# Performance work log

Measured on AMD Instinct MI355X. Metric: run time of the kernel, lower is better.

## Reference

```python
import jax, jax.numpy as jnp
import numpy as np


def _dw_conv(x, w, ks):
    # x: [1, B*k, H, W], w: [B*k, 1, ks, ks], groups = B*k depthwise conv
    pad = (ks - 1) // 2
    return jax.lax.conv_general_dilated(
        x, w, window_strides=(1, 1), padding=[(pad, pad), (pad, pad)],
        feature_group_count=x.shape[1],
        dimension_numbers=('NCHW', 'OIHW', 'NCHW'))


def setup_inputs() -> dict:
    key = jax.random.key(0)
    ks = jax.random.split(key, 12)
    B, Cin, M, O, H, W = 8, 256, 256, 256, 128, 128
    k = 128  # static top-k channel count (eval-mode: ceil(M * clamp(mean(scores),0.25,1.0)) ~ M/2)
    inp = {
        'x': jax.random.normal(ks[0], (B, Cin, H, W), jnp.float32),
        'pw1_w': jax.random.normal(ks[1], (M, Cin), jnp.float32) * 0.02,
        'pw1_b': jnp.zeros((M,), jnp.float32),
        'fc1_w': jax.random.normal(ks[2], (2 * M, M), jnp.float32) * 0.02,
        'fc1_b': jnp.zeros((2 * M,), jnp.float32),
        'fc2_w': jax.random.normal(ks[3], (M, 2 * M), jnp.float32) * 0.02,
        'fc2_b': jnp.zeros((M,), jnp.float32),
        'off_w': jax.random.normal(ks[4], (6, M), jnp.float32) * 0.02,
        'off_b': jnp.zeros((6,), jnp.float32),
        'dw3': jax.random.normal(ks[5], (M, 1, 3, 3), jnp.float32) * 0.1,
        'dw5': jax.random.normal(ks[6], (M, 1, 5, 5), jnp.float32) * 0.1,
        'dw7': jax.random.normal(ks[7], (M, 1, 7, 7), jnp.float32) * 0.1,
        'pw_w': jax.random.normal(ks[8], (O, 3 * M), jnp.float32) * 0.02,
        'pw_b': jnp.zeros((O,), jnp.float32),
        'k': k,
    }
    return inp


def reference(x, pw1_w, pw1_b, fc1_w, fc1_b, fc2_w, fc2_b, off_w, off_b,
              dw3, dw5, dw7, pw_w, pw_b, k):
    B, _, H, W = x.shape
    residual = x  # identity shortcut (stride=1, in==out)
    # pointwise_1 (1x1 conv)
    h = jnp.einsum('bchw,oc->bohw', x, pw1_w) + pw1_b[None, :, None, None]
    # WidthPredictor (eval mode): scores from GAP of pre-ReLU features
    gap = h.mean(axis=(2, 3))                                   # [B, M]
    hid = jax.nn.relu(gap @ fc1_w.T + fc1_b)
    scores = jax.nn.sigmoid(hid @ fc2_w.T + fc2_b)              # [B, M]
    _, idx = jax.lax.top_k(scores, k)                           # [B, k]
    mask = jnp.zeros_like(scores).at[jnp.arange(B)[:, None], idx].set(1.0)
    h = jax.nn.relu(h)
    # offset generator: GAP -> 1x1 conv -> tanh
    gap2 = h.mean(axis=(2, 3))
    offsets = jnp.tanh(gap2 @ off_w.T + off_b).reshape(B, 3, 2)  # [B, branches, 2]
    # mask then take first k channels (as in original: (x*mask)[:, :k])
    sel = (h * mask[:, :, None, None])[:, :k]                    # [B, k, H, W]
    conv_in = sel.reshape(1, B * k, H, W)
    outs = []
    for i, (ksz, base) in enumerate([(3, dw3), (5, dw5), (7, dw7)]):
        scale = jax.nn.sigmoid(offsets[:, i, 0]).reshape(B, 1, 1, 1, 1)
        shift = jnp.tanh(offsets[:, i, 1]).reshape(B, 1, 1, 1, 1)
        w = base[:k][None] * (1.0 + scale) + shift               # [B, k, 1, ks, ks]
        y = _dw_conv(conv_in, w.reshape(B * k, 1, ksz, ksz), ksz)
        outs.append(y.reshape(B, k, H, W))
    fused = jnp.concatenate(outs, axis=1)                        # [B, 3k, H, W]
    sel_pw = pw_w[:, :3 * k]                                     # [O, 3k]
    out = jnp.einsum('bchw,oc->bohw', fused, sel_pw) + pw_b[None, :, None, None]
    return out + residual
```

## Files before the change

### kernel.cpp

```cpp
#include <hip/hip_runtime.h>
#include <math.h>

constexpr int B  = 8;
constexpr int C  = 256;
constexpr int M  = 256;
constexpr int O  = 256;
constexpr int H  = 128;
constexpr int W  = 128;
constexpr int HW = H * W;
constexpr int K  = 128;

using f16  = _Float16;
using f16x8 = __attribute__((ext_vector_type(8))) _Float16;
using f32x4 = __attribute__((ext_vector_type(4))) float;

constexpr size_t WS_MEANX = 0;
constexpr size_t WS_MASK  = 2048;
constexpr size_t WS_G2    = 4096;
constexpr size_t WS_OFF   = 6144;
constexpr size_t WS_WE3   = 6208;
constexpr size_t WS_WE5   = 15424;
constexpr size_t WS_WE7   = 41024;
constexpr size_t WS_WT1F  = 91200;
constexpr size_t WS_WT2F  = 123968;
constexpr size_t WS_SELH  = 173120;
constexpr size_t WS_YH    = 8561728;

__global__ __launch_bounds__(256) void kA(const float* __restrict__ x,
                                          float* __restrict__ ws) {
  float* meanx   = ws + WS_MEANX;
  float* gap2sum = ws + WS_G2;
  int plane = blockIdx.x;
  const float* p = x + (size_t)plane * HW;
  float s = 0.f;
  for (int i = threadIdx.x; i < HW / 4; i += 256) {
    float4 v = ((const float4*)p)[i];
    s += v.x + v.y + v.z + v.w;
  }
  __shared__ float red[256];
  red[threadIdx.x] = s;
  __syncthreads();
  for (int off = 128; off > 0; off >>= 1) {
    if (threadIdx.x < off) red[threadIdx.x] += red[threadIdx.x + off];
    __syncthreads();
  }
  if (threadIdx.x == 0) meanx[plane] = red[0] * (1.f / HW);
  if (blockIdx.x < 8) gap2sum[blockIdx.x * 256 + threadIdx.x] = 0.f;
}

__global__ __launch_bounds__(256) void kT(const float* __restrict__ pw1_w,
                                          const float* __restrict__ pw_w,
                                          float* __restrict__ ws) {
  f16* wt1f = (f16*)(ws + WS_WT1F);
  f16* wt2f = (f16*)(ws + WS_WT2F);
  int t = blockIdx.x * 256 + threadIdx.x;
  if (t < C * M) wt1f[t] = (f16)pw1_w[t];
  if (t < 384 * O) {
    int o = t / 384, cc = t % 384;
    wt2f[t] = (f16)pw_w[(size_t)o * 768 + cc];
  }
}

__global__ __launch_bounds__(256) void kB(const float* __restrict__ pw1_w,
                                          const float* __restrict__ pw1_b,
                                          const float* __restrict__ fc1_w,
                                          const float* __restrict__ fc1_b,
                                          const float* __restrict__ fc2_w,
                                          const float* __restrict__ fc2_b,
                                          float* __restrict__ ws) {
  int b = blockIdx.x;
  const float* meanx = ws + WS_MEANX + b * C;
  float* maskg = ws + WS_MASK;
  __shared__ float s_gap[M];
  __shared__ float s_hid[512];
  __shared__ float s_sc[M];
  int t = threadIdx.x;
  int lane = t & 63, wv = t >> 6;

  float4 mx = ((const float4*)meanx)[lane];
  for (int o0 = wv * 64; o0 < wv * 64 + 64; o0 += 4) {
    float s[4];
#pragma unroll
    for (int j = 0; j < 4; j++) {
      float4 w = ((const float4*)(pw1_w + (size_t)(o0 + j) * C))[lane];
      s[j] = mx.x * w.x + mx.y * w.y + mx.z * w.z + mx.w * w.w;
    }
#pragma unroll
    for (int off = 32; off > 0; off >>= 1)
#pragma unroll
      for (int j = 0; j < 4; j++) s[j] += __shfl_xor(s[j], off, 64);
    if (lane == 0) {
#pragma unroll
      for (int j = 0; j < 4; j++) s_gap[o0 + j] = s[j] + pw1_b[o0 + j];
    }
  }
  __syncthreads();

  float4 g4 = ((const float4*)s_gap)[lane];
  for (int j0 = wv * 128; j0 < wv * 128 + 128; j0 += 4) {
    float s[4];
#pragma unroll
    for (int j = 0; j < 4; j++) {
      float4 w = ((const float4*)(fc1_w + (size_t)(j0 + j) * M))[lane];
      s[j] = g4.x * w.x + g4.y * w.y + g4.z * w.z + g4.w * w.w;
    }
#pragma unroll
    for (int off = 32; off > 0; off >>= 1)
#pragma unroll
      for (int j = 0; j < 4; j++) s[j] += __shfl_xor(s[j], off, 64);
    if (lane == 0) {
#pragma unroll
      for (int j = 0; j < 4; j++) {
        float v = s[j] + fc1_b[j0 + j];
        s_hid[j0 + j] = v > 0.f ? v : 0.f;
      }
    }
  }
  __syncthreads();

  float4 h0 = ((const float4*)s_hid)[lane];
  float4 h1 = ((const float4*)s_hid)[lane + 64];
  for (int o0 = wv * 64; o0 < wv * 64 + 64; o0 += 4) {
    float s[4];
#pragma unroll
    for (int j = 0; j < 4; j++) {
      const float4* wr = (const float4*)(fc2_w + (size_t)(o0 + j) * 512);
      float4 w0 = wr[lane];
      float4 w1 = wr[lane + 64];
      s[j] = h0.x * w0.x + h0.y * w0.y + h0.z * w0.z + h0.w * w0.w +
             h1.x * w1.x + h1.y * w1.y + h1.z * w1.z + h1.w * w1.w;
    }
#pragma unroll
    for (int off = 32; off > 0; off >>= 1)
#pragma unroll
      for (int j = 0; j < 4; j++) s[j] += __shfl_xor(s[j], off, 64);
    if (lane == 0) {
#pragma unroll
      for (int j = 0; j < 4; j++) {
        float v = s[j] + fc2_b[o0 + j];
        s_sc[o0 + j] = 1.f / (1.f + expf(-v));
      }
    }
  }
  __syncthreads();

  {
    int j = t;
    float sj = s_sc[j];
    int cnt = 0;
    for (int m = 0; m < M; m++) {
      float sm = s_sc[m];
      cnt += (sm > sj) || (sm == sj && m < j);
    }
    maskg[b * M + j] = (cnt < K) ? 1.f : 0.f;
  }
}

__global__ __launch_bounds__(256) void kCm(const float* __restrict__ x,
                                           const float* __restrict__ pw1_b,
                                           float* __restrict__ ws) {
  const f16* wt1f = (const f16*)(ws + WS_WT1F);
  float* gap2sum  = ws + WS_G2;
  f16* selh       = (f16*)(ws + WS_SELH);
  int b  = blockIdx.z;
  int p0 = blockIdx.x * 64;
  __shared__ f16 Af[256 * 32];
  __shared__ f16 Bf[64 * 32];

  int t = threadIdx.x, l = t & 63, w = t >> 6;
  int q = l >> 4, n = l & 15;
  const float* xb = x + (size_t)b * C * HW;

  f32x4 acc[4][4];
#pragma unroll
  for (int i = 0; i < 4; i++)
#pragma unroll
    for (int j = 0; j < 4; j++)
#pragma unroll
      for (int r = 0; r < 4; r++) acc[i][j][r] = 0.f;

  for (int k0 = 0; k0 < C; k0 += 32) {
#pragma unroll
    for (int i = 0; i < 4; i++) {
      int ch = t + i * 256;
      int mt = ch >> 6, qq = (ch >> 4) & 3, m = ch & 15;
      f16x8 v = *(const f16x8*)&wt1f[(size_t)(mt * 16 + m) * C + k0 + qq * 8];
      ((f16x8*)Af)[ch] = v;
    }
    {
      int ch = t;
      int nt = ch >> 6, qq = (ch >> 4) & 3, nn = ch & 15;
      int p = p0 + nt * 16 + nn;
      f16x8 fr;
#pragma unroll
      for (int j = 0; j < 8; j++)
        fr[j] = (f16)xb[(size_t)(k0 + qq * 8 + j) * HW + p];
      ((f16x8*)Bf)[ch] = fr;
    }
    __syncthreads();
    f16x8 bfr[4], afr[4];
#pragma unroll
    for (int nt = 0; nt < 4; nt++) bfr[nt] = ((const f16x8*)Bf)[nt * 64 + l];
#pragma unroll
    for (int mt = 0; mt < 4; mt++) afr[mt] = ((const f16x8*)Af)[(w * 4 + mt) * 64 + l];
#pragma unroll
    for (int mt = 0; mt < 4; mt++)
#pragma unroll
      for (int nt = 0; nt < 4; nt++)
        acc[mt][nt] = __builtin_amdgcn_mfma_f32_16x16x32_f16(afr[mt], bfr[nt],
                                                             acc[mt][nt], 0, 0, 0);
    __syncthreads();
  }

#pragma unroll
  for (int mt = 0; mt < 4; mt++) {
    float rsum[4] = {0.f, 0.f, 0.f, 0.f};
    int obase = w * 64 + mt * 16 + q * 4;
    float bias[4];
#pragma unroll
    for (int r = 0; r < 4; r++) bias[r] = pw1_b[obase + r];
#pragma unroll
    for (int nt = 0; nt < 4; nt++) {
      int p = p0 + nt * 16 + n;
#pragma unroll
      for (int r = 0; r < 4; r++) {
        float h = acc[mt][nt][r] + bias[r];
        h = h > 0.f ? h : 0.f;
        rsum[r] += h;
        int o = obase + r;
        if (o < K) selh[((size_t)(b * K + o)) * HW + p] = (f16)h;
      }
    }
#pragma unroll
    for (int off = 1; off < 16; off <<= 1)
#pragma unroll
      for (int r = 0; r < 4; r++) rsum[r] += __shfl_xor(rsum[r], off, 64);
    if (n == 0) {
#pragma unroll
      for (int r = 0; r < 4; r++)
        atomicAdd(&gap2sum[b * M + obase + r], rsum[r]);
    }
  }
}

__global__ __launch_bounds__(256) void kD1(const float* __restrict__ off_w,
                                           const float* __restrict__ off_b,
                                           float* __restrict__ ws) {
  const float* gap2sum = ws + WS_G2;
  float* offv = ws + WS_OFF;
  __shared__ float s_off[48];
  int t = threadIdx.x;
  int lane = t & 63, wv = t >> 6;
  for (int id = wv; id < 48; id += 4) {
    int b = id / 6, j = id % 6;
    float4 g = ((const float4*)(gap2sum + b * M))[lane];
    float4 w = ((const float4*)(off_w + (size_t)j * M))[lane];
    float s = (g.x * w.x + g.y * w.y + g.z * w.z + g.w * w.w) * (1.f / HW);
#pragma unroll
    for (int off = 32; off > 0; off >>= 1) s += __shfl_xor(s, off, 64);
    if (lane == 0) s_off[id] = tanhf(s + off_b[j]);
  }
  __syncthreads();
  if (t < 24) {
    int b = t / 3, i = t % 3;
    offv[t]      = 1.f + 1.f / (1.f + expf(-s_off[b * 6 + 2 * i]));
    offv[24 + t] = tanhf(s_off[b * 6 + 2 * i + 1]);
  }
}

__global__ __launch_bounds__(256) void kD2(const float* __restrict__ dw3,
                                           const float* __restrict__ dw5,
                                           const float* __restrict__ dw7,
                                           float* __restrict__ ws) {
  const float* offv  = ws + WS_OFF;
  const float* maskg = ws + WS_MASK;
  float* wE3 = ws + WS_WE3;
  float* wE5 = ws + WS_WE5;
  float* wE7 = ws + WS_WE7;
  int tid = blockIdx.x * 256 + threadIdx.x;
  int stride = gridDim.x * 256;
  for (int i = tid; i < B * K * 9; i += stride) {
    int b = i / (K * 9), rem = i % (K * 9), c = rem / 9;
    wE3[i] = (dw3[rem] * offv[b * 3 + 0] + offv[24 + b * 3 + 0]) * maskg[b * M + c];
  }
  for (int i = tid; i < B * K * 25; i += stride) {
    int b = i / (K * 25), rem = i % (K * 25), c = rem / 25;
    wE5[i] = (dw5[rem] * offv[b * 3 + 1] + offv[24 + b * 3 + 1]) * maskg[b * M + c];
  }
  for (int i = tid; i < B * K * 49; i += stride) {
    int b = i / (K * 49), rem = i % (K * 49), c = rem / 49;
    wE7[i] = (dw7[rem] * offv[b * 3 + 2] + offv[24 + b * 3 + 2]) * maskg[b * M + c];
  }
}

__global__ __launch_bounds__(256) void kEm(const float* __restrict__ ws_ro,
                                           float* __restrict__ ws) {
  constexpr int SH = 38, SW = 134;
  __shared__ float sm[SH][SW];
  const f16* selh = (const f16*)(ws_ro + WS_SELH);
  f16* yh         = (f16*)(ws + WS_YH);
  int blk = blockIdx.x;
  int chunk = blk & 3;
  int plane = blk >> 2;
  int b = plane >> 7, c = plane & 127;
  int r0 = chunk * 32;
  const f16* in = selh + (size_t)plane * HW;
  for (int i = threadIdx.x; i < SH * SW; i += 256) {
    int rr = i / SW, cc = i % SW;
    int gy = r0 - 3 + rr, gx = cc - 3;
    float v = 0.f;
    if (gy >= 0 && gy < H && gx >= 0 && gx < W) v = (float)in[gy * W + gx];
    sm[rr][cc] = v;
  }
  __syncthreads();
  int col   = threadIdx.x & 127;
  int rhalf = threadIdx.x >> 7;

  const float* wE[3] = {ws_ro + WS_WE3 + (size_t)plane * 9,
                        ws_ro + WS_WE5 + (size_t)plane * 25,
                        ws_ro + WS_WE7 + (size_t)plane * 49};

#define CONV_BRANCH(KS, BR)                                                    \
  {                                                                            \
    constexpr int P = (KS - 1) / 2;                                            \
    float w[KS * KS];                                                          \
    _Pragma("unroll") for (int i = 0; i < KS * KS; i++) w[i] = wE[BR][i];      \
    float acc[16];                                                             \
    _Pragma("unroll") for (int r = 0; r < 16; r++) acc[r] = 0.f;               \
    _Pragma("unroll") for (int iy = 0; iy < 16 + 2 * P; iy++) {                \
      float v[KS];                                                             \
      _Pragma("unroll") for (int dx = 0; dx < KS; dx++)                        \
          v[dx] = sm[rhalf * 16 + iy + (3 - P)][col + (3 - P) + dx];           \
      _Pragma("unroll") for (int rr = 0; rr < 16; rr++) {                      \
        int dy = iy - rr;                                                      \
        if (dy >= 0 && dy < KS) {                                              \
          _Pragma("unroll") for (int dx = 0; dx < KS; dx++)                    \
              acc[rr] += v[dx] * w[dy * KS + dx];                              \
        }                                                                      \
      }                                                                        \
    }                                                                          \
    f16* outp = yh + ((size_t)(BR * B + b) * K + c) * HW;                      \
    _Pragma("unroll") for (int rr = 0; rr < 16; rr++)                          \
        outp[(size_t)(r0 + rhalf * 16 + rr) * W + col] = (f16)acc[rr];         \
  }

  CONV_BRANCH(3, 0)
  CONV_BRANCH(5, 1)
  CONV_BRANCH(7, 2)
#undef CONV_BRANCH
}

__global__ __launch_bounds__(256) void kFm(const float* __restrict__ x,
                                           const float* __restrict__ pw_b,
                                           const float* __restrict__ ws,
                                           float* __restrict__ out) {
  const f16* wt2f = (const f16*)(ws + WS_WT2F);
  const f16* yh   = (const f16*)(ws + WS_YH);
  int b  = blockIdx.z;
  int p0 = blockIdx.x * 64;
  __shared__ f16 Af[256 * 32];
  __shared__ f16 Bf[64 * 32];

  int t = threadIdx.x, l = t & 63, w = t >> 6;
  int q = l >> 4, n = l & 15;

  f32x4 acc[4][4];
#pragma unroll
  for (int i = 0; i < 4; i++)
#pragma unroll
    for (int j = 0; j < 4; j++)
#pragma unroll
      for (int r = 0; r < 4; r++) acc[i][j][r] = 0.f;

  for (int k0 = 0; k0 < 384; k0 += 32) {
    int br = k0 >> 7, kk = k0 & 127;
    const f16* ybr = yh + (size_t)(br * B + b) * K * HW;
#pragma unroll
    for (int i = 0; i < 4; i++) {
      int ch = t + i * 256;
      int mt = ch >> 6, qq = (ch >> 4) & 3, m = ch & 15;
      f16x8 v = *(const f16x8*)&wt2f[(size_t)(mt * 16 + m) * 384 + k0 + qq * 8];
      ((f16x8*)Af)[ch] = v;
    }
    {
      int ch = t;
      int nt = ch >> 6, qq = (ch >> 4) & 3, nn = ch & 15;
      int p = p0 + nt * 16 + nn;
      f16x8 fr;
#pragma unroll
      for (int j = 0; j < 8; j++)
        fr[j] = ybr[(size_t)(kk + qq * 8 + j) * HW + p];
      ((f16x8*)Bf)[ch] = fr;
    }
    __syncthreads();
    f16x8 bfr[4], afr[4];
#pragma unroll
    for (int nt = 0; nt < 4; nt++) bfr[nt] = ((const f16x8*)Bf)[nt * 64 + l];
#pragma unroll
    for (int mt = 0; mt < 4; mt++) afr[mt] = ((const f16x8*)Af)[(w * 4 + mt) * 64 + l];
#pragma unroll
    for (int mt = 0; mt < 4; mt++)
#pragma unroll
      for (int nt = 0; nt < 4; nt++)
        acc[mt][nt] = __builtin_amdgcn_mfma_f32_16x16x32_f16(afr[mt], bfr[nt],
                                                             acc[mt][nt], 0, 0, 0);
    __syncthreads();
  }

#pragma unroll
  for (int mt = 0; mt < 4; mt++) {
    int obase = w * 64 + mt * 16 + q * 4;
    float bias[4];
#pragma unroll
    for (int r = 0; r < 4; r++) bias[r] = pw_b[obase + r];
#pragma unroll
    for (int nt = 0; nt < 4; nt++) {
      int p = p0 + nt * 16 + n;
#pragma unroll
      for (int r = 0; r < 4; r++) {
        size_t idx = ((size_t)b * O + obase + r) * HW + p;
        out[idx] = acc[mt][nt][r] + bias[r] + x[idx];
      }
    }
  }
}

extern "C" void kernel_launch(void* const* d_in, const int* in_sizes, int n_in,
                              void* d_out, int out_size, void* d_ws, size_t ws_size,
                              hipStream_t stream) {
  const float* x     = (const float*)d_in[0];
  const float* pw1_w = (const float*)d_in[1];
  const float* pw1_b = (const float*)d_in[2];
  const float* fc1_w = (const float*)d_in[3];
  const float* fc1_b = (const float*)d_in[4];
  const float* fc2_w = (const float*)d_in[5];
  const float* fc2_b = (const float*)d_in[6];
  const float* off_w = (const float*)d_in[7];
  const float* off_b = (const float*)d_in[8];
  const float* dw3   = (const float*)d_in[9];
  const float* dw5   = (const float*)d_in[10];
  const float* dw7   = (const float*)d_in[11];
  const float* pw_w  = (const float*)d_in[12];
  const float* pw_b  = (const float*)d_in[13];
  float* out = (float*)d_out;
  float* ws  = (float*)d_ws;

  kA<<<B * C, 256, 0, stream>>>(x, ws);
  kT<<<384, 256, 0, stream>>>(pw1_w, pw_w, ws);
  kB<<<B, 256, 0, stream>>>(pw1_w, pw1_b, fc1_w, fc1_b, fc2_w, fc2_b, ws);
  kCm<<<dim3(HW / 64, 1, B), 256, 0, stream>>>(x, pw1_b, ws);
  kD1<<<1, 256, 0, stream>>>(off_w, off_b, ws);
  kD2<<<84, 256, 0, stream>>>(dw3, dw5, dw7, ws);
  kEm<<<B * K * 4, 256, 0, stream>>>(ws, ws);
  kFm<<<dim3(HW / 64, 1, B), 256, 0, stream>>>(x, pw_b, ws, out);
}
```

Baseline: 649.4 us.

## Vectorize and prefetch GEMM tile loads into registers with swizzled B layout

Both pointwise GEMM kernels (kCm and kFm) now load the B operand with row-contiguous vector loads instead of strided scalar loads that walk channels. Tiles are stored to LDS in an XOR-swizzled layout and transposed on the LDS read side. The next k-slice of A and B is prefetched into registers while the MFMAs for the current slice run, a software pipeline that overlaps global latency with compute. The cost is scalar LDS reads for the B fragments and more register pressure.

```diff
diff --git a/kernel.cpp b/kernel.cpp
--- a/kernel.cpp
+++ b/kernel.cpp
@@ -171,6 +171,18 @@
   int q = l >> 4, n = l & 15;
   const float* xb = x + (size_t)b * C * HW;
 
+  int crow = t >> 3;
+  int oct  = t & 7;
+  int qc_s = (crow >> 3) & 3;
+  int posB = crow * 64 + (((oct >> 1) ^ qc_s) << 4) + (oct & 1) * 8;
+
+  int aoff[4];
+#pragma unroll
+  for (int i = 0; i < 4; i++) {
+    int ch = t + i * 256;
+    aoff[i] = ((ch >> 6) * 16 + (ch & 15)) * C + ((ch >> 4) & 3) * 8;
+  }
+
   f32x4 acc[4][4];
 #pragma unroll
   for (int i = 0; i < 4; i++)
@@ -179,28 +191,41 @@
 #pragma unroll
       for (int r = 0; r < 4; r++) acc[i][j][r] = 0.f;
 
+  f16x8 rA[4];
+  float4 rB0, rB1;
+  auto loadA = [&](int k0) {
+#pragma unroll
+    for (int i = 0; i < 4; i++) rA[i] = *(const f16x8*)&wt1f[aoff[i] + k0];
+  };
+  auto loadB = [&](int k0) {
+    const float* bs = xb + (size_t)(k0 + crow) * HW + p0 + oct * 8;
+    rB0 = ((const float4*)bs)[0];
+    rB1 = ((const float4*)bs)[1];
+  };
+  loadA(0);
+  loadB(0);
+
   for (int k0 = 0; k0 < C; k0 += 32) {
-#pragma unroll
-    for (int i = 0; i < 4; i++) {
-      int ch = t + i * 256;
-      int mt = ch >> 6, qq = (ch >> 4) & 3, m = ch & 15;
-      f16x8 v = *(const f16x8*)&wt1f[(size_t)(mt * 16 + m) * C + k0 + qq * 8];
-      ((f16x8*)Af)[ch] = v;
-    }
+    __syncthreads();
+#pragma unroll
+    for (int i = 0; i < 4; i++) ((f16x8*)Af)[t + i * 256] = rA[i];
     {
-      int ch = t;
-      int nt = ch >> 6, qq = (ch >> 4) & 3, nn = ch & 15;
-      int p = p0 + nt * 16 + nn;
-      f16x8 fr;
-#pragma unroll
-      for (int j = 0; j < 8; j++)
-        fr[j] = (f16)xb[(size_t)(k0 + qq * 8 + j) * HW + p];
-      ((f16x8*)Bf)[ch] = fr;
-    }
+      f16x8 bv;
+      bv[0] = (f16)rB0.x; bv[1] = (f16)rB0.y; bv[2] = (f16)rB0.z; bv[3] = (f16)rB0.w;
+      bv[4] = (f16)rB1.x; bv[5] = (f16)rB1.y; bv[6] = (f16)rB1.z; bv[7] = (f16)rB1.w;
+      *(f16x8*)&Bf[posB] = bv;
+    }
+    if (k0 + 32 < C) { loadA(k0 + 32); loadB(k0 + 32); }
     __syncthreads();
     f16x8 bfr[4], afr[4];
 #pragma unroll
-    for (int nt = 0; nt < 4; nt++) bfr[nt] = ((const f16x8*)Bf)[nt * 64 + l];
+    for (int nt = 0; nt < 4; nt++) {
+      f16x8 fr;
+#pragma unroll
+      for (int j = 0; j < 8; j++)
+        fr[j] = Bf[(q * 8 + j) * 64 + ((nt ^ q) << 4) + n];
+      bfr[nt] = fr;
+    }
 #pragma unroll
     for (int mt = 0; mt < 4; mt++) afr[mt] = ((const f16x8*)Af)[(w * 4 + mt) * 64 + l];
 #pragma unroll
@@ -209,7 +234,6 @@
       for (int nt = 0; nt < 4; nt++)
         acc[mt][nt] = __builtin_amdgcn_mfma_f32_16x16x32_f16(afr[mt], bfr[nt],
                                                              acc[mt][nt], 0, 0, 0);
-    __syncthreads();
   }
 
 #pragma unroll
@@ -364,6 +388,18 @@
   int t = threadIdx.x, l = t & 63, w = t >> 6;
   int q = l >> 4, n = l & 15;
 
+  int crow = t >> 3;
+  int oct  = t & 7;
+  int qc_s = (crow >> 3) & 3;
+  int posB = crow * 64 + (((oct >> 1) ^ qc_s) << 4) + (oct & 1) * 8;
+
+  int aoff[4];
+#pragma unroll
+  for (int i = 0; i < 4; i++) {
+    int ch = t + i * 256;
+    aoff[i] = ((ch >> 6) * 16 + (ch & 15)) * 384 + ((ch >> 4) & 3) * 8;
+  }
+
   f32x4 acc[4][4];
 #pragma unroll
   for (int i = 0; i < 4; i++)
@@ -372,30 +408,35 @@
 #pragma unroll
       for (int r = 0; r < 4; r++) acc[i][j][r] = 0.f;
 
-  for (int k0 = 0; k0 < 384; k0 += 32) {
+  f16x8 rA[4], rB;
+  auto loadA = [&](int k0) {
+#pragma unroll
+    for (int i = 0; i < 4; i++) rA[i] = *(const f16x8*)&wt2f[aoff[i] + k0];
+  };
+  auto loadB = [&](int k0) {
     int br = k0 >> 7, kk = k0 & 127;
     const f16* ybr = yh + (size_t)(br * B + b) * K * HW;
-#pragma unroll
-    for (int i = 0; i < 4; i++) {
-      int ch = t + i * 256;
-      int mt = ch >> 6, qq = (ch >> 4) & 3, m = ch & 15;
-      f16x8 v = *(const f16x8*)&wt2f[(size_t)(mt * 16 + m) * 384 + k0 + qq * 8];
-      ((f16x8*)Af)[ch] = v;
-    }
-    {
-      int ch = t;
-      int nt = ch >> 6, qq = (ch >> 4) & 3, nn = ch & 15;
-      int p = p0 + nt * 16 + nn;
-      f16x8 fr;
-#pragma unroll
-      for (int j = 0; j < 8; j++)
-        fr[j] = ybr[(size_t)(kk + qq * 8 + j) * HW + p];
-      ((f16x8*)Bf)[ch] = fr;
-    }
+    rB = *(const f16x8*)&ybr[(size_t)(kk + crow) * HW + p0 + oct * 8];
+  };
+  loadA(0);
+  loadB(0);
+
+  for (int k0 = 0; k0 < 384; k0 += 32) {
+    __syncthreads();
+#pragma unroll
+    for (int i = 0; i < 4; i++) ((f16x8*)Af)[t + i * 256] = rA[i];
+    *(f16x8*)&Bf[posB] = rB;
+    if (k0 + 32 < 384) { loadA(k0 + 32); loadB(k0 + 32); }
     __syncthreads();
     f16x8 bfr[4], afr[4];
 #pragma unroll
-    for (int nt = 0; nt < 4; nt++) bfr[nt] = ((const f16x8*)Bf)[nt * 64 + l];
+    for (int nt = 0; nt < 4; nt++) {
+      f16x8 fr;
+#pragma unroll
+      for (int j = 0; j < 8; j++)
+        fr[j] = Bf[(q * 8 + j) * 64 + ((nt ^ q) << 4) + n];
+      bfr[nt] = fr;
+    }
 #pragma unroll
     for (int mt = 0; mt < 4; mt++) afr[mt] = ((const f16x8*)Af)[(w * 4 + mt) * 64 + l];
 #pragma unroll
@@ -404,7 +445,6 @@
       for (int nt = 0; nt < 4; nt++)
         acc[mt][nt] = __builtin_amdgcn_mfma_f32_16x16x32_f16(afr[mt], bfr[nt],
                                                              acc[mt][nt], 0, 0, 0);
-    __syncthreads();
   }
 
 #pragma unroll
```

Result: no change. 647.2 us (-0.3%).

## Pre-pack GEMM operands into MFMA fragment layout and drop LDS staging

Applied to the files above, without the earlier changes.

Adds a kernel that transposes x into fp16 channel-interleaved blocks of 8 per pixel and computes the channel means with atomics, replacing the separate mean kernel. Weights are pre-swizzled into MFMA fragment order so both pointwise GEMMs load A and B fragments straight from global memory, with no shared-memory staging and no barriers. The depthwise conv kernel is rewritten to process 8 channels per block in fp16 LDS tiles and write its output in the same interleaved layout the second GEMM reads. The aim is to remove strided scalar loads and LDS round trips, at the cost of an extra transpose pass over x and a larger fp16 workspace.

```diff
diff --git a/kernel.cpp b/kernel.cpp
--- a/kernel.cpp
+++ b/kernel.cpp
@@ -10,7 +10,8 @@
 constexpr int HW = H * W;
 constexpr int K  = 128;
 
-using f16  = _Float16;
+using f16   = _Float16;
+using f16x2 = __attribute__((ext_vector_type(2))) _Float16;
 using f16x8 = __attribute__((ext_vector_type(8))) _Float16;
 using f32x4 = __attribute__((ext_vector_type(4))) float;
 
@@ -21,44 +22,57 @@
 constexpr size_t WS_WE3   = 6208;
 constexpr size_t WS_WE5   = 15424;
 constexpr size_t WS_WE7   = 41024;
-constexpr size_t WS_WT1F  = 91200;
-constexpr size_t WS_WT2F  = 123968;
+constexpr size_t WS_WT1G  = 91200;
+constexpr size_t WS_WT2G  = 123968;
 constexpr size_t WS_SELH  = 173120;
-constexpr size_t WS_YH    = 8561728;
-
-__global__ __launch_bounds__(256) void kA(const float* __restrict__ x,
-                                          float* __restrict__ ws) {
-  float* meanx   = ws + WS_MEANX;
-  float* gap2sum = ws + WS_G2;
-  int plane = blockIdx.x;
-  const float* p = x + (size_t)plane * HW;
-  float s = 0.f;
-  for (int i = threadIdx.x; i < HW / 4; i += 256) {
-    float4 v = ((const float4*)p)[i];
-    s += v.x + v.y + v.z + v.w;
-  }
-  __shared__ float red[256];
-  red[threadIdx.x] = s;
-  __syncthreads();
-  for (int off = 128; off > 0; off >>= 1) {
-    if (threadIdx.x < off) red[threadIdx.x] += red[threadIdx.x + off];
-    __syncthreads();
-  }
-  if (threadIdx.x == 0) meanx[plane] = red[0] * (1.f / HW);
-  if (blockIdx.x < 8) gap2sum[blockIdx.x * 256 + threadIdx.x] = 0.f;
-}
+constexpr size_t WS_BIG   = 8561728;
 
 __global__ __launch_bounds__(256) void kT(const float* __restrict__ pw1_w,
                                           const float* __restrict__ pw_w,
                                           float* __restrict__ ws) {
-  f16* wt1f = (f16*)(ws + WS_WT1F);
-  f16* wt2f = (f16*)(ws + WS_WT2F);
+  f16* wt1g = (f16*)(ws + WS_WT1G);
+  f16* wt2g = (f16*)(ws + WS_WT2G);
   int t = blockIdx.x * 256 + threadIdx.x;
-  if (t < C * M) wt1f[t] = (f16)pw1_w[t];
-  if (t < 384 * O) {
-    int o = t / 384, cc = t % 384;
-    wt2f[t] = (f16)pw_w[(size_t)o * 768 + cc];
-  }
+  if (t < 65536) {
+    int ks = t >> 13, fr = (t >> 9) & 15, l = (t >> 3) & 63, j = t & 7;
+    int o = fr * 16 + (l & 15);
+    int c = ks * 32 + ((l >> 4) << 3) + j;
+    wt1g[t] = (f16)pw1_w[o * C + c];
+  }
+  if (t < 98304) {
+    int ks = t >> 13, fr = (t >> 9) & 15, l = (t >> 3) & 63, j = t & 7;
+    int o = fr * 16 + (l & 15);
+    int cc = ks * 32 + ((l >> 4) << 3) + j;
+    wt2g[t] = (f16)pw_w[(size_t)o * 768 + cc];
+  }
+  if (t < 2048) {
+    ws[WS_MEANX + t] = 0.f;
+    ws[WS_G2 + t]    = 0.f;
+  }
+}
+
+__global__ __launch_bounds__(256) void kAT(const float* __restrict__ x,
+                                           float* __restrict__ ws) {
+  float* meanx = ws + WS_MEANX;
+  f16* xh      = (f16*)(ws + WS_BIG);
+  int b = blockIdx.z, ko = blockIdx.y, p0 = blockIdx.x * 256;
+  __shared__ float sx[8][256];
+  int t = threadIdx.x;
+  int c8 = t >> 5, pg = t & 31;
+  const float* xp = x + (size_t)(b * 256 + ko * 8 + c8) * HW + p0 + pg * 8;
+  float4 v0 = ((const float4*)xp)[0];
+  float4 v1 = ((const float4*)xp)[1];
+  *(float4*)&sx[c8][pg * 8]     = v0;
+  *(float4*)&sx[c8][pg * 8 + 4] = v1;
+  float s = v0.x + v0.y + v0.z + v0.w + v1.x + v1.y + v1.z + v1.w;
+#pragma unroll
+  for (int off = 16; off > 0; off >>= 1) s += __shfl_xor(s, off, 32);
+  if (pg == 0) atomicAdd(&meanx[b * 256 + ko * 8 + c8], s * (1.f / HW));
+  __syncthreads();
+  f16x8 o;
+#pragma unroll
+  for (int j = 0; j < 8; j++) o[j] = (f16)sx[j][t];
+  *(f16x8*)&xh[((size_t)(b * 32 + ko) * HW + p0 + t) * 8] = o;
 }
 
 __global__ __launch_bounds__(256) void kB(const float* __restrict__ pw1_w,
@@ -156,20 +170,17 @@
   }
 }
 
-__global__ __launch_bounds__(256) void kCm(const float* __restrict__ x,
-                                           const float* __restrict__ pw1_b,
+__global__ __launch_bounds__(256) void kCm(const float* __restrict__ pw1_b,
                                            float* __restrict__ ws) {
-  const f16* wt1f = (const f16*)(ws + WS_WT1F);
+  const f16* wt1g = (const f16*)(ws + WS_WT1G);
+  const f16* xh   = (const f16*)(ws + WS_BIG);
   float* gap2sum  = ws + WS_G2;
   f16* selh       = (f16*)(ws + WS_SELH);
   int b  = blockIdx.z;
   int p0 = blockIdx.x * 64;
-  __shared__ f16 Af[256 * 32];
-  __shared__ f16 Bf[64 * 32];
 
   int t = threadIdx.x, l = t & 63, w = t >> 6;
   int q = l >> 4, n = l & 15;
-  const float* xb = x + (size_t)b * C * HW;
 
   f32x4 acc[4][4];
 #pragma unroll
@@ -179,37 +190,24 @@
 #pragma unroll
       for (int r = 0; r < 4; r++) acc[i][j][r] = 0.f;
 
-  for (int k0 = 0; k0 < C; k0 += 32) {
-#pragma unroll
-    for (int i = 0; i < 4; i++) {
-      int ch = t + i * 256;
-      int mt = ch >> 6, qq = (ch >> 4) & 3, m = ch & 15;
-      f16x8 v = *(const f16x8*)&wt1f[(size_t)(mt * 16 + m) * C + k0 + qq * 8];
-      ((f16x8*)Af)[ch] = v;
-    }
-    {
-      int ch = t;
-      int nt = ch >> 6, qq = (ch >> 4) & 3, nn = ch & 15;
-      int p = p0 + nt * 16 + nn;
-      f16x8 fr;
-#pragma unroll
-      for (int j = 0; j < 8; j++)
-        fr[j] = (f16)xb[(size_t)(k0 + qq * 8 + j) * HW + p];
-      ((f16x8*)Bf)[ch] = fr;
-    }
-    __syncthreads();
-    f16x8 bfr[4], afr[4];
-#pragma unroll
-    for (int nt = 0; nt < 4; nt++) bfr[nt] = ((const f16x8*)Bf)[nt * 64 + l];
-#pragma unroll
-    for (int mt = 0; mt < 4; mt++) afr[mt] = ((const f16x8*)Af)[(w * 4 + mt) * 64 + l];
+  const f16* bbase = xh + (size_t)(b * 32 + q) * (HW * 8) + (size_t)(p0 + n) * 8;
+  const f16* abase = wt1g + (size_t)(w * 4) * 512 + (size_t)l * 8;
+
+#pragma unroll 2
+  for (int ks = 0; ks < 8; ks++) {
+    f16x8 afr[4], bfr[4];
+#pragma unroll
+    for (int mt = 0; mt < 4; mt++)
+      afr[mt] = *(const f16x8*)(abase + (size_t)(ks * 16 + mt) * 512);
+#pragma unroll
+    for (int nt = 0; nt < 4; nt++)
+      bfr[nt] = *(const f16x8*)(bbase + (size_t)ks * (4 * HW * 8) + nt * 128);
 #pragma unroll
     for (int mt = 0; mt < 4; mt++)
 #pragma unroll
       for (int nt = 0; nt < 4; nt++)
         acc[mt][nt] = __builtin_amdgcn_mfma_f32_16x16x32_f16(afr[mt], bfr[nt],
                                                              acc[mt][nt], 0, 0, 0);
-    __syncthreads();
   }
 
 #pragma unroll
@@ -295,58 +293,68 @@
 
 __global__ __launch_bounds__(256) void kEm(const float* __restrict__ ws_ro,
                                            float* __restrict__ ws) {
-  constexpr int SH = 38, SW = 134;
-  __shared__ float sm[SH][SW];
+  __shared__ f16 sm[8 * 22 * 72];
   const f16* selh = (const f16*)(ws_ro + WS_SELH);
-  f16* yh         = (f16*)(ws + WS_YH);
-  int blk = blockIdx.x;
-  int chunk = blk & 3;
-  int plane = blk >> 2;
-  int b = plane >> 7, c = plane & 127;
-  int r0 = chunk * 32;
-  const f16* in = selh + (size_t)plane * HW;
-  for (int i = threadIdx.x; i < SH * SW; i += 256) {
-    int rr = i / SW, cc = i % SW;
-    int gy = r0 - 3 + rr, gx = cc - 3;
-    float v = 0.f;
-    if (gy >= 0 && gy < H && gx >= 0 && gx < W) v = (float)in[gy * W + gx];
-    sm[rr][cc] = v;
-  }
-  __syncthreads();
-  int col   = threadIdx.x & 127;
-  int rhalf = threadIdx.x >> 7;
-
-  const float* wE[3] = {ws_ro + WS_WE3 + (size_t)plane * 9,
-                        ws_ro + WS_WE5 + (size_t)plane * 25,
-                        ws_ro + WS_WE7 + (size_t)plane * 49};
-
-#define CONV_BRANCH(KS, BR)                                                    \
+  f16* yh2        = (f16*)(ws + WS_BIG);
+  int bx = blockIdx.x;
+  int slab = bx >> 1, chalf = bx & 1;
+  int ko = blockIdx.y, b = blockIdx.z;
+  int r0 = slab * 16, c0 = chalf * 64;
+
+  for (int i = threadIdx.x; i < 8 * 1584; i += 256) {
+    int chn = i / 1584, rem = i - chn * 1584;
+    int rr = rem / 72, cc = rem - rr * 72;
+    int gy = r0 - 3 + rr, gx = c0 - 3 + cc;
+    f16 v = (f16)0.f;
+    if (gy >= 0 && gy < H && gx >= 0 && gx < W)
+      v = selh[(size_t)(b * 128 + ko * 8 + chn) * HW + gy * W + gx];
+    sm[i] = v;
+  }
+  __syncthreads();
+
+  int t = threadIdx.x;
+  int ch = t & 7, cp = t >> 3;
+  int cglob = c0 + cp * 2;
+
+#define CONV_BRANCH(KS, BR, WSOFF, NW, WSHIFT)                                 \
   {                                                                            \
     constexpr int P = (KS - 1) / 2;                                            \
+    const float* wp = ws_ro + WSOFF + (size_t)(b * 128 + ko * 8 + ch) * (KS*KS); \
     float w[KS * KS];                                                          \
-    _Pragma("unroll") for (int i = 0; i < KS * KS; i++) w[i] = wE[BR][i];      \
-    float acc[16];                                                             \
-    _Pragma("unroll") for (int r = 0; r < 16; r++) acc[r] = 0.f;               \
+    _Pragma("unroll") for (int i = 0; i < KS * KS; i++) w[i] = wp[i];          \
+    float a0[16], a1[16];                                                      \
+    _Pragma("unroll") for (int r = 0; r < 16; r++) { a0[r] = 0.f; a1[r] = 0.f; } \
     _Pragma("unroll") for (int iy = 0; iy < 16 + 2 * P; iy++) {                \
-      float v[KS];                                                             \
-      _Pragma("unroll") for (int dx = 0; dx < KS; dx++)                        \
-          v[dx] = sm[rhalf * 16 + iy + (3 - P)][col + (3 - P) + dx];           \
+      int hr = iy + 3 - P;                                                     \
+      const f16x2* rowp = (const f16x2*)(sm + ch * 1584 + hr * 72);            \
+      float vv[2 * NW];                                                        \
+      _Pragma("unroll") for (int u = 0; u < NW; u++) {                         \
+        f16x2 pr = rowp[cp + WSHIFT + u];                                      \
+        vv[2 * u]     = (float)pr[0];                                          \
+        vv[2 * u + 1] = (float)pr[1];                                          \
+      }                                                                        \
       _Pragma("unroll") for (int rr = 0; rr < 16; rr++) {                      \
         int dy = iy - rr;                                                      \
         if (dy >= 0 && dy < KS) {                                              \
-          _Pragma("unroll") for (int dx = 0; dx < KS; dx++)                    \
-              acc[rr] += v[dx] * w[dy * KS + dx];                              \
+          _Pragma("unroll") for (int dx = 0; dx < KS; dx++) {                  \
+            int m = (3 - P) + dx - 2 * WSHIFT;                                 \
+            a0[rr] += vv[m]     * w[dy * KS + dx];                             \
+            a1[rr] += vv[m + 1] * w[dy * KS + dx];                             \
+          }                                                                    \
         }                                                                      \
       }                                                                        \
     }                                                                          \
-    f16* outp = yh + ((size_t)(BR * B + b) * K + c) * HW;                      \
-    _Pragma("unroll") for (int rr = 0; rr < 16; rr++)                          \
-        outp[(size_t)(r0 + rhalf * 16 + rr) * W + col] = (f16)acc[rr];         \
-  }
-
-  CONV_BRANCH(3, 0)
-  CONV_BRANCH(5, 1)
-  CONV_BRANCH(7, 2)
+    f16* op = yh2 + (size_t)(b * 48 + BR * 16 + ko) * HW * 8;                  \
+    _Pragma("unroll") for (int rr = 0; rr < 16; rr++) {                        \
+      size_t pa = ((size_t)(r0 + rr) * W + cglob) * 8 + ch;                    \
+      op[pa]     = (f16)a0[rr];                                                \
+      op[pa + 8] = (f16)a1[rr];                                                \
+    }                                                                          \
+  }
+
+  CONV_BRANCH(3, 0, WS_WE3, 2, 1)
+  CONV_BRANCH(5, 1, WS_WE5, 4, 0)
+  CONV_BRANCH(7, 2, WS_WE7, 4, 0)
 #undef CONV_BRANCH
 }
 
@@ -354,12 +362,10 @@
                                            const float* __restrict__ pw_b,
                                            const float* __restrict__ ws,
                                            float* __restrict__ out) {
-  const f16* wt2f = (const f16*)(ws + WS_WT2F);
-  const f16* yh   = (const f16*)(ws + WS_YH);
+  const f16* wt2g = (const f16*)(ws + WS_WT2G);
+  const f16* yh2  = (const f16*)(ws + WS_BIG);
   int b  = blockIdx.z;
   int p0 = blockIdx.x * 64;
-  __shared__ f16 Af[256 * 32];
-  __shared__ f16 Bf[64 * 32];
 
   int t = threadIdx.x, l = t & 63, w = t >> 6;
   int q = l >> 4, n = l & 15;
@@ -372,39 +378,24 @@
 #pragma unroll
       for (int r = 0; r < 4; r++) acc[i][j][r] = 0.f;
 
-  for (int k0 = 0; k0 < 384; k0 += 32) {
-    int br = k0 >> 7, kk = k0 & 127;
-    const f16* ybr = yh + (size_t)(br * B + b) * K * HW;
-#pragma unroll
-    for (int i = 0; i < 4; i++) {
-      int ch = t + i * 256;
-      int mt = ch >> 6, qq = (ch >> 4) & 3, m = ch & 15;
-      f16x8 v = *(const f16x8*)&wt2f[(size_t)(mt * 16 + m) * 384 + k0 + qq * 8];
-      ((f16x8*)Af)[ch] = v;
-    }
-    {
-      int ch = t;
-      int nt = ch >> 6, qq = (ch >> 4) & 3, nn = ch & 15;
-      int p = p0 + nt * 16 + nn;
-      f16x8 fr;
-#pragma unroll
-      for (int j = 0; j < 8; j++)
-        fr[j] = ybr[(size_t)(kk + qq * 8 + j) * HW + p];
-      ((f16x8*)Bf)[ch] = fr;
-    }
-    __syncthreads();
-    f16x8 bfr[4], afr[4];
-#pragma unroll
-    for (int nt = 0; nt < 4; nt++) bfr[nt] = ((const f16x8*)Bf)[nt * 64 + l];
-#pragma unroll
-    for (int mt = 0; mt < 4; mt++) afr[mt] = ((const f16x8*)Af)[(w * 4 + mt) * 64 + l];
+  const f16* bbase = yh2 + (size_t)(b * 48 + q) * (HW * 8) + (size_t)(p0 + n) * 8;
+  const f16* abase = wt2g + (size_t)(w * 4) * 512 + (size_t)l * 8;
+
+#pragma unroll 2
+  for (int ks = 0; ks < 12; ks++) {
+    f16x8 afr[4], bfr[4];
+#pragma unroll
+    for (int mt = 0; mt < 4; mt++)
+      afr[mt] = *(const f16x8*)(abase + (size_t)(ks * 16 + mt) * 512);
+#pragma unroll
+    for (int nt = 0; nt < 4; nt++)
+      bfr[nt] = *(const f16x8*)(bbase + (size_t)ks * (4 * HW * 8) + nt * 128);
 #pragma unroll
     for (int mt = 0; mt < 4; mt++)
 #pragma unroll
       for (int nt = 0; nt < 4; nt++)
         acc[mt][nt] = __builtin_amdgcn_mfma_f32_16x16x32_f16(afr[mt], bfr[nt],
                                                              acc[mt][nt], 0, 0, 0);
-    __syncthreads();
   }
 
 #pragma unroll
@@ -445,12 +436,12 @@
   float* out = (float*)d_out;
   float* ws  = (float*)d_ws;
 
-  kA<<<B * C, 256, 0, stream>>>(x, ws);
   kT<<<384, 256, 0, stream>>>(pw1_w, pw_w, ws);
+  kAT<<<dim3(HW / 256, 32, B), 256, 0, stream>>>(x, ws);
   kB<<<B, 256, 0, stream>>>(pw1_w, pw1_b, fc1_w, fc1_b, fc2_w, fc2_b, ws);
-  kCm<<<dim3(HW / 64, 1, B), 256, 0, stream>>>(x, pw1_b, ws);
+  kCm<<<dim3(HW / 64, 1, B), 256, 0, stream>>>(pw1_b, ws);
   kD1<<<1, 256, 0, stream>>>(off_w, off_b, ws);
   kD2<<<84, 256, 0, stream>>>(dw3, dw5, dw7, ws);
-  kEm<<<B * K * 4, 256, 0, stream>>>(ws, ws);
+  kEm<<<dim3(16, 16, B), 256, 0, stream>>>(ws, ws);
   kFm<<<dim3(HW / 64, 1, B), 256, 0, stream>>>(x, pw_b, ws, out);
 }
```

New measurement: 622.3 us. -4.2%, faster.
